# Performance work log

Measured on AMD Instinct MI355X. Metric: run time of the kernel, lower is better.

The kernel has to match this reference:

```python
import jax, jax.numpy as jnp
import numpy as np

TGT_LEN, BS, SRC_LEN, VOCAB, DIM, EMB = 24, 16, 400, 32000, 256, 256


def setup_inputs() -> dict:
    key = jax.random.key(0)
    ks = jax.random.split(key, 16)
    g = lambda k, s, sc: jax.random.normal(k, s, dtype=jnp.float32) * sc
    return {
        "inputs": jax.random.randint(ks[0], (TGT_LEN, BS), 0, VOCAB),
        "src": jax.random.randint(ks[1], (SRC_LEN, BS), 0, VOCAB),
        "h_e": g(ks[2], (SRC_LEN, BS, DIM), 0.1),
        "h0": g(ks[3], (BS, DIM), 0.1),
        "c0": g(ks[4], (BS, DIM), 0.1),
        "W_emb": g(ks[5], (VOCAB, EMB), 0.05),
        "W_ih": g(ks[6], (4 * DIM, EMB), 0.05),
        "b_ih": g(ks[7], (4 * DIM,), 0.05),
        "W_hh": g(ks[8], (4 * DIM, DIM), 0.05),
        "b_hh": g(ks[9], (4 * DIM,), 0.05),
        "W_attn_enc": g(ks[10], (DIM, DIM), 0.05),
        "W_attn_dec": g(ks[11], (DIM, DIM), 0.05),
        "W_proj": g(ks[12], (EMB, 3 * DIM), 0.05),
        "W_u": g(ks[13], (1, 3 * DIM), 0.05),
        "b_u": g(ks[14], (1,), 0.05),
        "b_out": g(ks[15], (VOCAB, 1), 0.05),
        "pad_id": 1,
    }


def reference(inputs, src, h_e, h0, c0, W_emb, W_ih, b_ih, W_hh, b_hh,
              W_attn_enc, W_attn_dec, W_proj, W_u, b_u, b_out, pad_id):
    tgt_len, bs = inputs.shape
    vocab = W_emb.shape[0]
    dim = h0.shape[1]

    emb_seq = W_emb[inputs]                       # [T, bs, emb]
    # weight-shared output projection (sect 2.4), loop-invariant -> hoisted
    W_out = jnp.tanh(W_emb @ W_proj)              # [vocab, 3*dim]
    b_out_v = b_out[:, 0]                         # [vocab]
    w_u = W_u[0]                                  # [3*dim]
    src_ids = src.T                               # [bs, src_len]
    rows = jnp.arange(bs)[:, None]
    pos = jnp.arange(tgt_len)

    def lstm_cell(x, h, c):
        gates = x @ W_ih.T + b_ih + h @ W_hh.T + b_hh
        i, f, g_, o = jnp.split(gates, 4, axis=1)
        c_new = jax.nn.sigmoid(f) * c + jax.nn.sigmoid(i) * jnp.tanh(g_)
        h_new = jax.nn.sigmoid(o) * jnp.tanh(c_new)
        return h_new, c_new

    def step(carry, xs):
        h, c, E_hist, hd_hist = carry
        emb_t, t = xs
        h, c = lstm_cell(emb_t, h, c)
        hd_t = h                                   # [bs, dim]
        # --- temporal encoder intra-attention (eq. 3-5) ---
        q = hd_t @ W_attn_enc                      # [bs, dim]
        expE = jnp.exp(jnp.einsum('bd,sbd->bs', q, h_e))  # [bs, src]
        EE = jnp.where(t == 0, expE, expE / E_hist)
        E_hist = jnp.where(t == 0, expE, E_hist + expE)
        A_e = EE / EE.sum(axis=1, keepdims=True)
        c_e = jnp.einsum('bs,sbd->bd', A_e, h_e)
        # --- decoder intra-attention over hd_history (includes current step) ---
        hd_hist = hd_hist.at[t].set(hd_t)          # [T, bs, dim]
        qd = hd_t @ W_attn_dec
        Ed = jnp.einsum('bd,tbd->bt', qd, hd_hist)
        mask = pos[None, :] <= t
        EEd = jnp.where(mask, jnp.exp(Ed), 0.0)
        A_d = EEd / EEd.sum(axis=1, keepdims=True)
        cd = jnp.einsum('bt,tbd->bd', A_d, hd_hist)
        cd_t = jnp.where(t == 0, jnp.zeros_like(cd), cd)  # t==0: cd is zeros
        # --- pointer-generator (sect 2.3) ---
        feat = jnp.concatenate([hd_t, c_e, cd_t], axis=1)   # [bs, 3*dim]
        p_switch = jax.nn.sigmoid(feat @ w_u + b_u[0])       # [bs]
        logits = feat @ W_out.T + b_out_v                     # [bs, vocab]
        logits = logits.at[:, pad_id].set(-jnp.inf)
        p_gen = jax.nn.softmax(logits, axis=1)
        copy = jnp.zeros((bs, vocab), logits.dtype).at[rows, src_ids].add(A_e)
        scores_t = (copy + p_gen) * p_switch[:, None]
        return (h, c, E_hist, hd_hist), scores_t

    hd_hist0 = jnp.zeros((tgt_len, bs, dim), h0.dtype)
    E_hist0 = jnp.ones((bs, h_e.shape[0]), h0.dtype)
    _, scores = jax.lax.scan(step, (h0, c0, E_hist0, hd_hist0), (emb_seq, pos))
    return scores  # [T, bs, vocab] mixed copy/gen distribution per step
```

## Files before the change

kernel.cpp:

```cpp
#include <hip/hip_runtime.h>
#include <cstdint>
#include <cstddef>

#define TGT   24
#define BS    16
#define SRC   400
#define VOCABN 32000
#define DIM   256
#define NROW  (TGT*BS)
#define LSTM_NBLK 4

typedef __bf16 bf16_t;
typedef __bf16 v8bf __attribute__((ext_vector_type(8)));
typedef float  v4f  __attribute__((ext_vector_type(4)));

__device__ __forceinline__ float fast_tanh(float x) {
    float e = __expf(2.f*x);
    return 1.f - 2.f/(e + 1.f);
}

__global__ void k_prep(const float* __restrict__ Whh, const float* __restrict__ Wad,
                       const float* __restrict__ he,  const float* __restrict__ Wemb,
                       const float* __restrict__ Wproj, const float* __restrict__ Wae,
                       const float* __restrict__ Wih, const int* __restrict__ inputs,
                       const float* __restrict__ h0,
                       bf16_t* o_whh, bf16_t* o_wadT, bf16_t* o_he, bf16_t* o_heT,
                       bf16_t* o_wae, bf16_t* o_wih, bf16_t* o_wprojT, bf16_t* o_embA,
                       bf16_t* o_hhi, bf16_t* o_hlo)
{
    const long S0=262144, S1=65536, S2=1638400, S3=1638400, S4=65536, S5=262144, S6=196608, S7=98304, S8=4096;
    const long total = S0+S1+S2+S3+S4+S5+S6+S7+S8;
    for (long i = (long)blockIdx.x*blockDim.x + threadIdx.x; i < total;
         i += (long)gridDim.x*blockDim.x) {
        long j = i;
        if (j < S0) { o_whh[j] = (bf16_t)Whh[j]; continue; }           j -= S0;
        if (j < S1) { long n = j>>8, k = j&255; o_wadT[j] = (bf16_t)Wad[k*DIM + n]; continue; } j -= S1;
        if (j < S2) { o_he[j] = (bf16_t)he[j]; continue; }             j -= S2;
        if (j < S3) {
            long b = j / 102400, rem = j % 102400, d = rem / 400, s = rem % 400;
            o_heT[j] = (bf16_t)he[(s*BS + b)*DIM + d]; continue; }     j -= S3;
        if (j < S4) { o_wae[j] = (bf16_t)Wae[j]; continue; }           j -= S4;
        if (j < S5) { o_wih[j] = (bf16_t)Wih[j]; continue; }           j -= S5;
        if (j < S6) { long n = j>>8, k = j&255; o_wprojT[j] = (bf16_t)Wproj[k*768 + n]; continue; } j -= S6;
        if (j < S7) { long r = j>>8, k = j&255; o_embA[j] = (bf16_t)Wemb[(long)inputs[r]*DIM + k]; continue; } j -= S7;
        {
          float v = h0[j];
          bf16_t hi = (bf16_t)v;
          o_hhi[j] = hi; o_hlo[j] = (bf16_t)(v - (float)hi); }
    }
}

__device__ __forceinline__ void gemm_tile(
    const int tid, bf16_t* As, bf16_t* Bs,
    const bf16_t* __restrict__ A, const float* __restrict__ A32,
    const bf16_t* __restrict__ B,
    const int tileIdx, const int N, const int K, const int Ntiles, const int mode,
    float* __restrict__ outF, bf16_t* __restrict__ outB,
    const float* __restrict__ bias0, const float* __restrict__ bias1,
    const int* __restrict__ padp, float* __restrict__ rsum)
{
    const int mt   = tileIdx / Ntiles, nt = tileIdx % Ntiles;
    const int m0   = mt*128, n0 = nt*128;
    const int lane = tid & 63, wave = tid >> 6;
    const int wm   = wave >> 1, wn = wave & 1;
    const int quad = lane >> 4, l16 = lane & 15;

    v4f acc[4][4];
#pragma unroll
    for (int i=0;i<4;i++)
#pragma unroll
        for (int j=0;j<4;j++) acc[i][j] = (v4f){0.f,0.f,0.f,0.f};

    const int srow = tid >> 1, shalf = tid & 1;
    const bf16_t* Ag   = A   ? A   + (size_t)(m0+srow)*K + shalf*16 : nullptr;
    const float*  Ag32 = A32 ? A32 + (size_t)(m0+srow)*K + shalf*16 : nullptr;
    const bf16_t* Bg = B + (size_t)(n0+srow)*K + shalf*16;
    bf16_t* AsW = &As[srow*40 + shalf*16];
    bf16_t* BsW = &Bs[srow*40 + shalf*16];

    for (int kc = 0; kc < K; kc += 32) {
        __syncthreads();
        uint4 b0 = *(const uint4*)(Bg + kc);
        uint4 b1 = *(const uint4*)(Bg + kc + 8);
        if (A32) {
            float4 f0 = *(const float4*)(Ag32 + kc);
            float4 f1 = *(const float4*)(Ag32 + kc + 4);
            float4 f2 = *(const float4*)(Ag32 + kc + 8);
            float4 f3 = *(const float4*)(Ag32 + kc + 12);
            v8bf u0, u1;
            u0[0]=(bf16_t)f0.x; u0[1]=(bf16_t)f0.y; u0[2]=(bf16_t)f0.z; u0[3]=(bf16_t)f0.w;
            u0[4]=(bf16_t)f1.x; u0[5]=(bf16_t)f1.y; u0[6]=(bf16_t)f1.z; u0[7]=(bf16_t)f1.w;
            u1[0]=(bf16_t)f2.x; u1[1]=(bf16_t)f2.y; u1[2]=(bf16_t)f2.z; u1[3]=(bf16_t)f2.w;
            u1[4]=(bf16_t)f3.x; u1[5]=(bf16_t)f3.y; u1[6]=(bf16_t)f3.z; u1[7]=(bf16_t)f3.w;
            *(v8bf*)AsW = u0; *(v8bf*)(AsW+8) = u1;
        } else {
            uint4 a0 = *(const uint4*)(Ag + kc);
            uint4 a1 = *(const uint4*)(Ag + kc + 8);
            *(uint4*)AsW = a0; *(uint4*)(AsW+8) = a1;
        }
        *(uint4*)BsW = b0; *(uint4*)(BsW+8) = b1;
        __syncthreads();
        v8bf af[4], bb[4];
#pragma unroll
        for (int i=0;i<4;i++) {
            af[i] = *(const v8bf*)&As[(wm*64 + i*16 + l16)*40 + quad*8];
            bb[i] = *(const v8bf*)&Bs[(wn*64 + i*16 + l16)*40 + quad*8];
        }
#pragma unroll
        for (int i=0;i<4;i++)
#pragma unroll
            for (int j=0;j<4;j++)
                acc[i][j] = __builtin_amdgcn_mfma_f32_16x16x32_bf16(af[i], bb[j], acc[i][j], 0,0,0);
    }

    const int pad = padp ? *padp : -1;
    float* rs = (float*)As;
    if (mode == 3) {
        __syncthreads();
        if (tid < 128) rs[tid] = 0.f;
        __syncthreads();
    }
#pragma unroll
    for (int i=0;i<4;i++) {
        float rloc[4] = {0.f,0.f,0.f,0.f};
#pragma unroll
        for (int j=0;j<4;j++) {
#pragma unroll
            for (int r=0;r<4;r++) {
                const int gr = m0 + wm*64 + i*16 + quad*4 + r;
                const int gc = n0 + wn*64 + j*16 + l16;
                const float v = acc[i][j][r];
                if (mode == 0)      outF[(size_t)gr*N + gc] = v + bias0[gc] + bias1[gc];
                else if (mode == 1) outB[(size_t)gr*N + gc] = (bf16_t)fast_tanh(v);
                else if (mode == 2) outB[(size_t)gr*N + gc] = (bf16_t)v;
                else if (mode == 4) outF[(size_t)gr*N + (gc & 255)*4 + (gc >> 8)] = v + bias0[gc] + bias1[gc];
                else {
                    float ex = (gc == pad) ? 0.f : __expf(v + bias0[gc]);
                    outF[(size_t)gr*N + gc] = ex;
                    rloc[r] += ex;
                }
            }
        }
        if (mode == 3) {
#pragma unroll
            for (int r=0;r<4;r++)
                atomicAdd(&rs[wm*64 + i*16 + quad*4 + r], rloc[r]);
        }
    }
    if (mode == 3) {
        __syncthreads();
        if (tid < 128) atomicAdd(&rsum[m0 + tid], rs[tid]);
    }
}

__global__ __launch_bounds__(256) void k_gemm(
    const bf16_t* __restrict__ A, const float* __restrict__ A32,
    const bf16_t* __restrict__ B,
    int M, int N, int K, int Ntiles, int mode,
    float* outF, bf16_t* outB,
    const float* __restrict__ bias0, const float* __restrict__ bias1,
    const int* __restrict__ padp, float* __restrict__ rsum)
{
    (void)M;
    __shared__ bf16_t As[128*40];
    __shared__ bf16_t Bs[128*40];
    gemm_tile(threadIdx.x, As, Bs, A, A32, B, blockIdx.x, N, K, Ntiles, mode,
              outF, outB, bias0, bias1, padp, rsum);
}

__global__ __launch_bounds__(256) void k_gemm2(
    const bf16_t* __restrict__ embA, const bf16_t* __restrict__ wih,
    float* __restrict__ xg, const float* __restrict__ b_ih, const float* __restrict__ b_hh,
    const bf16_t* __restrict__ heA, const bf16_t* __restrict__ waeB, bf16_t* __restrict__ keB)
{
    __shared__ bf16_t As[128*40];
    __shared__ bf16_t Bs[128*40];
    if (blockIdx.x < 24)
        gemm_tile(threadIdx.x, As, Bs, embA, nullptr, wih, blockIdx.x, 1024, 256, 8, 4,
                  xg, nullptr, b_ih, b_hh, nullptr, nullptr);
    else
        gemm_tile(threadIdx.x, As, Bs, heA, nullptr, waeB, blockIdx.x - 24, 256, 256, 2, 2,
                  nullptr, keB, nullptr, nullptr, nullptr, nullptr);
}

__device__ __forceinline__ void gridbar(int* bar, int target) {
    __syncthreads();
    if (threadIdx.x == 0) {
        __threadfence();
        __hip_atomic_fetch_add(bar, 1, __ATOMIC_ACQ_REL, __HIP_MEMORY_SCOPE_AGENT);
        while (__hip_atomic_load(bar, __ATOMIC_ACQUIRE, __HIP_MEMORY_SCOPE_AGENT) < target) { }
        __threadfence();
    }
    __syncthreads();
}

__global__ __launch_bounds__(512, 2) void k_lstm(
    const bf16_t* __restrict__ Whh, const float* __restrict__ xgT,
    const float* __restrict__ c0,
    bf16_t* __restrict__ hhiG, bf16_t* __restrict__ hloG,
    float* __restrict__ hallF, bf16_t* __restrict__ hallB,
    int* __restrict__ bar)
{
    __shared__ float gl[16][260];

    const int tid = threadIdx.x;
    const int k = blockIdx.x;
    const int w = tid >> 6, lane = tid & 63;
    const int l16 = lane & 15, quad = lane >> 4;

    v8bf wb[2][8];
#pragma unroll
    for (int ct = 0; ct < 2; ++ct) {
        const int c = w*32 + ct*16 + l16;
        const int row = (c >> 6)*256 + k*64 + (c & 63);
#pragma unroll
        for (int kc = 0; kc < 8; ++kc)
            wb[ct][kc] = *(const v8bf*)&Whh[(size_t)row*DIM + kc*32 + quad*8];
    }

    float cst[2];
#pragma unroll
    for (int e = 0; e < 2; ++e) {
        const int li = tid + e*512;
        cst[e] = c0[(li >> 6)*DIM + k*64 + (li & 63)];
    }

    for (int step = 0; step < TGT; ++step) {
        v8bf ahi[8], alo[8];
#pragma unroll
        for (int kc = 0; kc < 8; ++kc) {
            ahi[kc] = *(const v8bf*)&hhiG[l16*DIM + kc*32 + quad*8];
            alo[kc] = *(const v8bf*)&hloG[l16*DIM + kc*32 + quad*8];
        }
        float4 xv[2];
#pragma unroll
        for (int e = 0; e < 2; ++e) {
            const int li = tid + e*512;
            const int b = li >> 6, dd = li & 63;
            xv[e] = *(const float4*)&xgT[((size_t)(step*BS + b)*DIM + k*64 + dd)*4];
        }

        v4f acc[2] = {(v4f){0.f,0.f,0.f,0.f}, (v4f){0.f,0.f,0.f,0.f}};
#pragma unroll
        for (int kc = 0; kc < 8; ++kc)
#pragma unroll
            for (int ct = 0; ct < 2; ++ct) {
                acc[ct] = __builtin_amdgcn_mfma_f32_16x16x32_bf16(ahi[kc], wb[ct][kc], acc[ct], 0,0,0);
                acc[ct] = __builtin_amdgcn_mfma_f32_16x16x32_bf16(alo[kc], wb[ct][kc], acc[ct], 0,0,0);
            }
#pragma unroll
        for (int ct = 0; ct < 2; ++ct) {
            const int c = w*32 + ct*16 + l16;
#pragma unroll
            for (int r = 0; r < 4; ++r)
                gl[quad*4 + r][c] = acc[ct][r];
        }
        __syncthreads();
#pragma unroll
        for (int e = 0; e < 2; ++e) {
            const int li = tid + e*512;
            const int b = li >> 6, dd = li & 63;
            const int d = k*64 + dd;
            const float gi = gl[b][dd]        + xv[e].x;
            const float gf = gl[b][64 + dd]   + xv[e].y;
            const float gg = gl[b][128 + dd]  + xv[e].z;
            const float go = gl[b][192 + dd]  + xv[e].w;
            const float si = 1.f/(1.f+__expf(-gi));
            const float sf = 1.f/(1.f+__expf(-gf));
            const float so = 1.f/(1.f+__expf(-go));
            const float cn = sf*cst[e] + si*fast_tanh(gg);
            const float hn = so*fast_tanh(cn);
            cst[e] = cn;
            const bf16_t hi = (bf16_t)hn;
            hhiG[b*DIM + d] = hi;
            hloG[b*DIM + d] = (bf16_t)(hn - (float)hi);
            hallF[(size_t)(step*BS + b)*DIM + d] = hn;
            hallB[(size_t)(step*BS + b)*DIM + d] = hi;
        }
        if (step < TGT-1) gridbar(bar, (step+1)*LSTM_NBLK);
    }
}

__device__ __forceinline__ void escore_body(const int blk, const int tid, float* hS,
    const bf16_t* __restrict__ ke, const float* __restrict__ hallF, float* __restrict__ expE)
{
    const int t = blk >> 4, b = blk & 15;
    hS[tid] = hallF[(size_t)(t*BS + b)*DIM + tid];
    __syncthreads();
    for (int s = tid; s < SRC; s += 256) {
        const v8bf* kp = (const v8bf*)(ke + ((size_t)s*BS + b)*DIM);
        float e = 0.f;
#pragma unroll 8
        for (int m=0;m<32;m++) {
            v8bf kv = kp[m];
#pragma unroll
            for (int i=0;i<8;i++) e += (float)kv[i]*hS[m*8+i];
        }
        expE[((size_t)t*BS + b)*SRC + s] = __expf(e);
    }
}

__global__ __launch_bounds__(256) void k_esq(
    const bf16_t* __restrict__ ke, const float* __restrict__ hallF, float* __restrict__ expE,
    const bf16_t* __restrict__ hallB, const bf16_t* __restrict__ wadT, bf16_t* __restrict__ qdG)
{
    __shared__ __align__(16) char shb[20480];
    if (blockIdx.x < NROW) {
        escore_body(blockIdx.x, threadIdx.x, (float*)shb, ke, hallF, expE);
        return;
    }
    gemm_tile(threadIdx.x, (bf16_t*)shb, (bf16_t*)(shb + 10240), hallB, nullptr, wadT,
              blockIdx.x - NROW, 256, 256, 2, 2, nullptr, qdG, nullptr, nullptr, nullptr, nullptr);
}

__device__ void attn_body(char* sh, const int blk, const int tid,
    const float* __restrict__ expE, const bf16_t* __restrict__ heT,
    const float* __restrict__ hallF, const bf16_t* __restrict__ qdG,
    const float* __restrict__ wu, const float* __restrict__ bu,
    bf16_t* __restrict__ feat, float* __restrict__ Ae, float* __restrict__ ps)
{
    float* hS   = (float*)sh;
    float* qdS  = hS + 256;
    float* eeS  = qdS + 256;
    float* adS  = eeS + 400;
    float* red  = adS + 24;
    float* misc = red + 4;
    const int t = blk >> 4, b = blk & 15;

    hS[tid]  = hallF[(size_t)(t*BS + b)*DIM + tid];
    qdS[tid] = (float)qdG[(size_t)(t*BS + b)*DIM + tid];
    __syncthreads();

    for (int s = tid; s < SRC; s += 256) {
        float prev = 0.f;
        for (int tp = 0; tp < t; ++tp) prev += expE[((size_t)tp*BS + b)*SRC + s];
        float my = expE[((size_t)t*BS + b)*SRC + s];
        eeS[s] = (t == 0) ? my : my / prev;
    }
    __syncthreads();
    {
        float pa = 0.f;
        for (int s = tid; s < SRC; s += 256) pa += eeS[s];
#pragma unroll
        for (int o=32;o>0;o>>=1) pa += __shfl_down(pa, o);
        if ((tid & 63) == 0) red[tid>>6] = pa;
        __syncthreads();
        if (tid == 0) misc[0] = 1.f/(red[0]+red[1]+red[2]+red[3]);
        __syncthreads();
    }
    const float inv_es = misc[0];
    for (int s = tid; s < SRC; s += 256)
        Ae[((size_t)t*BS + b)*SRC + s] = eeS[s] * inv_es;

    float ce;
    {
        const v8bf* hp = (const v8bf*)(heT + ((size_t)b*DIM + tid)*SRC);
        float acc = 0.f;
#pragma unroll 10
        for (int m=0;m<50;m++) {
            v8bf hv = hp[m];
#pragma unroll
            for (int i=0;i<8;i++) acc += (float)hv[i]*eeS[m*8+i];
        }
        ce = acc * inv_es;
    }

    {
        const int wv = tid >> 6, ln = tid & 63;
        for (int tau = wv; tau <= t; tau += 4) {
            float4 a = *(const float4*)(hallF + ((size_t)(tau*BS + b))*DIM + ln*4);
            float e = a.x*qdS[ln*4] + a.y*qdS[ln*4+1] + a.z*qdS[ln*4+2] + a.w*qdS[ln*4+3];
#pragma unroll
            for (int o=32;o>0;o>>=1) e += __shfl_down(e, o);
            if (ln == 0) adS[tau] = __expf(e);
        }
    }
    __syncthreads();
    if (tid < 64) {
        float v = (tid <= t) ? adS[tid] : 0.f;
#pragma unroll
        for (int o=32;o>0;o>>=1) v += __shfl_down(v, o);
        if (tid == 0) misc[1] = 1.f/v;
    }
    __syncthreads();
    float cd = 0.f;
    for (int tau = 0; tau <= t; ++tau)
        cd += adS[tau] * hallF[((size_t)(tau*BS + b))*DIM + tid];
    cd *= misc[1];
    if (t == 0) cd = 0.f;

    const float hd = hS[tid];
    const size_t fr = ((size_t)t*BS + b)*768;
    feat[fr + tid]       = (bf16_t)hd;
    feat[fr + 256 + tid] = (bf16_t)ce;
    feat[fr + 512 + tid] = (bf16_t)cd;
    float pw = hd*wu[tid] + ce*wu[256 + tid] + cd*wu[512 + tid];
#pragma unroll
    for (int o=32;o>0;o>>=1) pw += __shfl_down(pw, o);
    if ((tid & 63) == 0) red[tid>>6] = pw;
    __syncthreads();
    if (tid == 0) {
        float s = red[0]+red[1]+red[2]+red[3];
        ps[t*BS + b] = 1.f/(1.f+__expf(-(s + bu[0])));
    }
}

__global__ __launch_bounds__(256) void k_attnw(
    const float* __restrict__ expE, const bf16_t* __restrict__ heT,
    const float* __restrict__ hallF, const bf16_t* __restrict__ qdG,
    const float* __restrict__ wu, const float* __restrict__ bu,
    bf16_t* __restrict__ feat, float* __restrict__ Ae, float* __restrict__ ps,
    const float* __restrict__ Wemb, const bf16_t* __restrict__ wprojT,
    bf16_t* __restrict__ woutB)
{
    __shared__ __align__(16) char shb[20480];
    if (blockIdx.x < NROW) {
        attn_body(shb, blockIdx.x, threadIdx.x, expE, heT, hallF, qdG, wu, bu, feat, Ae, ps);
        return;
    }
    gemm_tile(threadIdx.x, (bf16_t*)shb, (bf16_t*)(shb + 10240), nullptr, Wemb, wprojT,
              blockIdx.x - NROW, 768, 256, 6, 1,
              nullptr, woutB, nullptr, nullptr, nullptr, nullptr);
}

__global__ __launch_bounds__(256) void k_final(
    float* __restrict__ out, const float* __restrict__ rsum,
    const float* __restrict__ ps, const int* __restrict__ src,
    const float* __restrict__ Ae)
{
    const int r = blockIdx.x;
    const int b = r & (BS-1);
    const float p  = ps[r];
    const float sc = p / rsum[r];
    float4* o4 = (float4*)(out + (size_t)r*VOCABN);
    for (int i = threadIdx.x; i < VOCABN/4; i += 256) {
        float4 v = o4[i];
        v.x*=sc; v.y*=sc; v.z*=sc; v.w*=sc;
        o4[i] = v;
    }
    __syncthreads();
    for (int s = threadIdx.x; s < SRC; s += 256) {
        const int v = src[s*BS + b];
        atomicAdd(&out[(size_t)r*VOCABN + v], Ae[(size_t)r*SRC + s] * p);
    }
}

#define O_WHH    0u
#define O_WADT   524288u
#define O_HEBF   655360u
#define O_HET    3932160u
#define O_KE     7208960u
#define O_WAE    10485760u
#define O_WPROJT 10616832u
#define O_WIH    11010048u
#define O_EMBA   11534336u
#define O_WOUT   11730944u
#define O_XG     60882944u
#define O_HALLF  62455808u
#define O_HALLB  62849024u
#define O_QD     63045632u
#define O_EXPE   63242240u
#define O_FEAT   63856640u
#define O_AE     64446464u
#define O_PS     65060864u
#define O_BAR    65062400u
#define O_RSUM   65063936u

extern "C" void kernel_launch(void* const* d_in, const int* in_sizes, int n_in,
                              void* d_out, int out_size, void* d_ws, size_t ws_size,
                              hipStream_t stream)
{
    const int*   inputs = (const int*)  d_in[0];
    const int*   src    = (const int*)  d_in[1];
    const float* h_e    = (const float*)d_in[2];
    const float* h0     = (const float*)d_in[3];
    const float* c0     = (const float*)d_in[4];
    const float* W_emb  = (const float*)d_in[5];
    const float* W_ih   = (const float*)d_in[6];
    const float* b_ih   = (const float*)d_in[7];
    const float* W_hh   = (const float*)d_in[8];
    const float* b_hh   = (const float*)d_in[9];
    const float* W_ae   = (const float*)d_in[10];
    const float* W_ad   = (const float*)d_in[11];
    const float* W_proj = (const float*)d_in[12];
    const float* W_u    = (const float*)d_in[13];
    const float* b_u    = (const float*)d_in[14];
    const float* b_out  = (const float*)d_in[15];
    const int*   pad_id = (const int*)  d_in[16];

    char* w = (char*)d_ws;
    bf16_t* whh_bf  = (bf16_t*)(w + O_WHH);
    bf16_t* wadT_bf = (bf16_t*)(w + O_WADT);
    bf16_t* he_bf   = (bf16_t*)(w + O_HEBF);
    bf16_t* heT_bf  = (bf16_t*)(w + O_HET);
    bf16_t* ke_bf   = (bf16_t*)(w + O_KE);
    bf16_t* wae_bf  = (bf16_t*)(w + O_WAE);
    bf16_t* wprojT  = (bf16_t*)(w + O_WPROJT);
    bf16_t* wih_bf  = (bf16_t*)(w + O_WIH);
    bf16_t* embA_bf = (bf16_t*)(w + O_EMBA);
    bf16_t* wout_bf = (bf16_t*)(w + O_WOUT);
    float*  xg      = (float*) (w + O_XG);
    float*  hallF   = (float*) (w + O_HALLF);
    bf16_t* hallB   = (bf16_t*)(w + O_HALLB);
    bf16_t* qdG     = (bf16_t*)(w + O_QD);
    float*  expE    = (float*) (w + O_EXPE);
    bf16_t* hhiG    = (bf16_t*)(w + O_EXPE);
    bf16_t* hloG    = (bf16_t*)(w + O_EXPE + 8192);
    bf16_t* feat_bf = (bf16_t*)(w + O_FEAT);
    float*  Ae      = (float*) (w + O_AE);
    float*  ps      = (float*) (w + O_PS);
    int*    bar     = (int*)   (w + O_BAR);
    float*  rsum    = (float*) (w + O_RSUM);
    float*  out     = (float*)d_out;

    k_prep<<<1024, 256, 0, stream>>>(W_hh, W_ad, h_e, W_emb, W_proj, W_ae, W_ih, inputs, h0,
                                     whh_bf, wadT_bf, he_bf, heT_bf,
                                     wae_bf, wih_bf, wprojT, embA_bf, hhiG, hloG);
    hipMemsetAsync(w + O_BAR, 0, 3072, stream);
    k_gemm2<<<124, 256, 0, stream>>>(embA_bf, wih_bf, xg, b_ih, b_hh,
                                     he_bf, wae_bf, ke_bf);
    k_lstm<<<LSTM_NBLK, 512, 0, stream>>>(whh_bf, xg, c0, hhiG, hloG,
                                          hallF, hallB, bar);
    k_esq<<<NROW + 6, 256, 0, stream>>>(ke_bf, hallF, expE, hallB, wadT_bf, qdG);
    k_attnw<<<NROW + 1500, 256, 0, stream>>>(expE, heT_bf, hallF, qdG, W_u, b_u,
                                             feat_bf, Ae, ps,
                                             W_emb, wprojT, wout_bf);
    k_gemm<<<750, 256, 0, stream>>>(feat_bf, nullptr, wout_bf, NROW, VOCABN, 768, 250, 3,
                                    out, nullptr, b_out, nullptr, pad_id, rsum);
    k_final<<<NROW, 256, 0, stream>>>(out, rsum, ps, src, Ae);
}
```

Measured before the change: 448.6 us.

## Precompute temporal attention prefix sums and specialize vocab GEMM with K=64 tiles

New measurement: 436.9 us. -2.6%, faster.

```diff
diff --git a/kernel.cpp b/kernel.cpp
--- a/kernel.cpp
+++ b/kernel.cpp
@@ -13,6 +13,7 @@
 typedef __bf16 bf16_t;
 typedef __bf16 v8bf __attribute__((ext_vector_type(8)));
 typedef float  v4f  __attribute__((ext_vector_type(4)));
+typedef unsigned int u32;
 
 __device__ __forceinline__ float fast_tanh(float x) {
     float e = __expf(2.f*x);
@@ -56,8 +57,7 @@
     const bf16_t* __restrict__ B,
     const int tileIdx, const int N, const int K, const int Ntiles, const int mode,
     float* __restrict__ outF, bf16_t* __restrict__ outB,
-    const float* __restrict__ bias0, const float* __restrict__ bias1,
-    const int* __restrict__ padp, float* __restrict__ rsum)
+    const float* __restrict__ bias0, const float* __restrict__ bias1)
 {
     const int mt   = tileIdx / Ntiles, nt = tileIdx % Ntiles;
     const int m0   = mt*128, n0 = nt*128;
@@ -113,16 +113,8 @@
                 acc[i][j] = __builtin_amdgcn_mfma_f32_16x16x32_bf16(af[i], bb[j], acc[i][j], 0,0,0);
     }
 
-    const int pad = padp ? *padp : -1;
-    float* rs = (float*)As;
-    if (mode == 3) {
-        __syncthreads();
-        if (tid < 128) rs[tid] = 0.f;
-        __syncthreads();
-    }
 #pragma unroll
     for (int i=0;i<4;i++) {
-        float rloc[4] = {0.f,0.f,0.f,0.f};
 #pragma unroll
         for (int j=0;j<4;j++) {
 #pragma unroll
@@ -134,38 +126,9 @@
                 else if (mode == 1) outB[(size_t)gr*N + gc] = (bf16_t)fast_tanh(v);
                 else if (mode == 2) outB[(size_t)gr*N + gc] = (bf16_t)v;
                 else if (mode == 4) outF[(size_t)gr*N + (gc & 255)*4 + (gc >> 8)] = v + bias0[gc] + bias1[gc];
-                else {
-                    float ex = (gc == pad) ? 0.f : __expf(v + bias0[gc]);
-                    outF[(size_t)gr*N + gc] = ex;
-                    rloc[r] += ex;
-                }
             }
         }
-        if (mode == 3) {
-#pragma unroll
-            for (int r=0;r<4;r++)
-                atomicAdd(&rs[wm*64 + i*16 + quad*4 + r], rloc[r]);
-        }
-    }
-    if (mode == 3) {
-        __syncthreads();
-        if (tid < 128) atomicAdd(&rsum[m0 + tid], rs[tid]);
-    }
-}
-
-__global__ __launch_bounds__(256) void k_gemm(
-    const bf16_t* __restrict__ A, const float* __restrict__ A32,
-    const bf16_t* __restrict__ B,
-    int M, int N, int K, int Ntiles, int mode,
-    float* outF, bf16_t* outB,
-    const float* __restrict__ bias0, const float* __restrict__ bias1,
-    const int* __restrict__ padp, float* __restrict__ rsum)
-{
-    (void)M;
-    __shared__ bf16_t As[128*40];
-    __shared__ bf16_t Bs[128*40];
-    gemm_tile(threadIdx.x, As, Bs, A, A32, B, blockIdx.x, N, K, Ntiles, mode,
-              outF, outB, bias0, bias1, padp, rsum);
+    }
 }
 
 __global__ __launch_bounds__(256) void k_gemm2(
@@ -177,10 +140,94 @@
     __shared__ bf16_t Bs[128*40];
     if (blockIdx.x < 24)
         gemm_tile(threadIdx.x, As, Bs, embA, nullptr, wih, blockIdx.x, 1024, 256, 8, 4,
-                  xg, nullptr, b_ih, b_hh, nullptr, nullptr);
+                  xg, nullptr, b_ih, b_hh);
     else
         gemm_tile(threadIdx.x, As, Bs, heA, nullptr, waeB, blockIdx.x - 24, 256, 256, 2, 2,
-                  nullptr, keB, nullptr, nullptr, nullptr, nullptr);
+                  nullptr, keB, nullptr, nullptr);
+}
+
+__global__ __launch_bounds__(256) void k_gemm3(
+    const bf16_t* __restrict__ A, const bf16_t* __restrict__ B,
+    float* __restrict__ outF, const float* __restrict__ bias0,
+    const int* __restrict__ padp, float* __restrict__ rsum)
+{
+    __shared__ bf16_t As[128*72];
+    __shared__ bf16_t Bs[128*72];
+    const int tid = threadIdx.x;
+    const int mt = blockIdx.x / 250, nt = blockIdx.x % 250;
+    const int m0 = mt*128, n0 = nt*128;
+    const int lane = tid & 63, wave = tid >> 6;
+    const int wm = wave >> 1, wn = wave & 1;
+    const int quad = lane >> 4, l16 = lane & 15;
+
+    v4f acc[4][4];
+#pragma unroll
+    for (int i=0;i<4;i++)
+#pragma unroll
+        for (int j=0;j<4;j++) acc[i][j] = (v4f){0.f,0.f,0.f,0.f};
+
+    const int srow = tid >> 1, shalf = tid & 1;
+    const bf16_t* Ag = A + (size_t)(m0+srow)*768 + shalf*32;
+    const bf16_t* Bg = B + (size_t)(n0+srow)*768 + shalf*32;
+    bf16_t* AsW = &As[srow*72 + shalf*32];
+    bf16_t* BsW = &Bs[srow*72 + shalf*32];
+
+    for (int kc = 0; kc < 768; kc += 64) {
+        __syncthreads();
+        uint4 a0 = *(const uint4*)(Ag + kc);
+        uint4 a1 = *(const uint4*)(Ag + kc + 8);
+        uint4 a2 = *(const uint4*)(Ag + kc + 16);
+        uint4 a3 = *(const uint4*)(Ag + kc + 24);
+        uint4 b0 = *(const uint4*)(Bg + kc);
+        uint4 b1 = *(const uint4*)(Bg + kc + 8);
+        uint4 b2 = *(const uint4*)(Bg + kc + 16);
+        uint4 b3 = *(const uint4*)(Bg + kc + 24);
+        *(uint4*)(AsW)    = a0; *(uint4*)(AsW+8)  = a1;
+        *(uint4*)(AsW+16) = a2; *(uint4*)(AsW+24) = a3;
+        *(uint4*)(BsW)    = b0; *(uint4*)(BsW+8)  = b1;
+        *(uint4*)(BsW+16) = b2; *(uint4*)(BsW+24) = b3;
+        __syncthreads();
+#pragma unroll
+        for (int kk = 0; kk < 2; ++kk) {
+            v8bf af[4], bb[4];
+#pragma unroll
+            for (int i=0;i<4;i++) {
+                af[i] = *(const v8bf*)&As[(wm*64 + i*16 + l16)*72 + kk*32 + quad*8];
+                bb[i] = *(const v8bf*)&Bs[(wn*64 + i*16 + l16)*72 + kk*32 + quad*8];
+            }
+#pragma unroll
+            for (int i=0;i<4;i++)
+#pragma unroll
+                for (int j=0;j<4;j++)
+                    acc[i][j] = __builtin_amdgcn_mfma_f32_16x16x32_bf16(af[i], bb[j], acc[i][j], 0,0,0);
+        }
+    }
+
+    const int pad = *padp;
+    float* rs = (float*)As;
+    __syncthreads();
+    if (tid < 128) rs[tid] = 0.f;
+    __syncthreads();
+#pragma unroll
+    for (int i=0;i<4;i++) {
+        float rloc[4] = {0.f,0.f,0.f,0.f};
+#pragma unroll
+        for (int j=0;j<4;j++) {
+#pragma unroll
+            for (int r=0;r<4;r++) {
+                const int gr = m0 + wm*64 + i*16 + quad*4 + r;
+                const int gc = n0 + wn*64 + j*16 + l16;
+                const float ex = (gc == pad) ? 0.f : __expf(acc[i][j][r] + bias0[gc]);
+                outF[(size_t)gr*VOCABN + gc] = ex;
+                rloc[r] += ex;
+            }
+        }
+#pragma unroll
+        for (int r=0;r<4;r++)
+            atomicAdd(&rs[wm*64 + i*16 + quad*4 + r], rloc[r]);
+    }
+    __syncthreads();
+    if (tid < 128) atomicAdd(&rsum[m0 + tid], rs[tid]);
 }
 
 __device__ __forceinline__ void gridbar(int* bar, int target) {
@@ -310,11 +357,24 @@
         return;
     }
     gemm_tile(threadIdx.x, (bf16_t*)shb, (bf16_t*)(shb + 10240), hallB, nullptr, wadT,
-              blockIdx.x - NROW, 256, 256, 2, 2, nullptr, qdG, nullptr, nullptr, nullptr, nullptr);
+              blockIdx.x - NROW, 256, 256, 2, 2, nullptr, qdG, nullptr, nullptr);
+}
+
+__global__ __launch_bounds__(256) void k_prefix(float* __restrict__ expE)
+{
+    const int i = blockIdx.x*256 + threadIdx.x;
+    if (i >= BS*SRC) return;
+    const int b = i / SRC, s = i % SRC;
+    float c = 0.f;
+    for (int t = 0; t < TGT; ++t) {
+        const size_t idx = ((size_t)t*BS + b)*SRC + s;
+        c += expE[idx];
+        expE[idx] = c;
+    }
 }
 
 __device__ void attn_body(char* sh, const int blk, const int tid,
-    const float* __restrict__ expE, const bf16_t* __restrict__ heT,
+    const float* __restrict__ cumE, const bf16_t* __restrict__ heT,
     const float* __restrict__ hallF, const bf16_t* __restrict__ qdG,
     const float* __restrict__ wu, const float* __restrict__ bu,
     bf16_t* __restrict__ feat, float* __restrict__ Ae, float* __restrict__ ps)
@@ -332,10 +392,13 @@
     __syncthreads();
 
     for (int s = tid; s < SRC; s += 256) {
-        float prev = 0.f;
-        for (int tp = 0; tp < t; ++tp) prev += expE[((size_t)tp*BS + b)*SRC + s];
-        float my = expE[((size_t)t*BS + b)*SRC + s];
-        eeS[s] = (t == 0) ? my : my / prev;
+        if (t == 0) {
+            eeS[s] = cumE[(size_t)b*SRC + s];
+        } else {
+            const float prev = cumE[((size_t)(t-1)*BS + b)*SRC + s];
+            const float cur  = cumE[((size_t)t*BS + b)*SRC + s];
+            eeS[s] = (cur - prev) / prev;
+        }
     }
     __syncthreads();
     {
@@ -406,7 +469,7 @@
 }
 
 __global__ __launch_bounds__(256) void k_attnw(
-    const float* __restrict__ expE, const bf16_t* __restrict__ heT,
+    const float* __restrict__ cumE, const bf16_t* __restrict__ heT,
     const float* __restrict__ hallF, const bf16_t* __restrict__ qdG,
     const float* __restrict__ wu, const float* __restrict__ bu,
     bf16_t* __restrict__ feat, float* __restrict__ Ae, float* __restrict__ ps,
@@ -415,12 +478,12 @@
 {
     __shared__ __align__(16) char shb[20480];
     if (blockIdx.x < NROW) {
-        attn_body(shb, blockIdx.x, threadIdx.x, expE, heT, hallF, qdG, wu, bu, feat, Ae, ps);
+        attn_body(shb, blockIdx.x, threadIdx.x, cumE, heT, hallF, qdG, wu, bu, feat, Ae, ps);
         return;
     }
     gemm_tile(threadIdx.x, (bf16_t*)shb, (bf16_t*)(shb + 10240), nullptr, Wemb, wprojT,
               blockIdx.x - NROW, 768, 256, 6, 1,
-              nullptr, woutB, nullptr, nullptr, nullptr, nullptr);
+              nullptr, woutB, nullptr, nullptr);
 }
 
 __global__ __launch_bounds__(256) void k_final(
@@ -522,10 +585,10 @@
     k_lstm<<<LSTM_NBLK, 512, 0, stream>>>(whh_bf, xg, c0, hhiG, hloG,
                                           hallF, hallB, bar);
     k_esq<<<NROW + 6, 256, 0, stream>>>(ke_bf, hallF, expE, hallB, wadT_bf, qdG);
+    k_prefix<<<25, 256, 0, stream>>>(expE);
     k_attnw<<<NROW + 1500, 256, 0, stream>>>(expE, heT_bf, hallF, qdG, W_u, b_u,
                                              feat_bf, Ae, ps,
                                              W_emb, wprojT, wout_bf);
-    k_gemm<<<750, 256, 0, stream>>>(feat_bf, nullptr, wout_bf, NROW, VOCABN, 768, 250, 3,
-                                    out, nullptr, b_out, nullptr, pad_id, rsum);
+    k_gemm3<<<750, 256, 0, stream>>>(feat_bf, wout_bf, out, b_out, pad_id, rsum);
     k_final<<<NROW, 256, 0, stream>>>(out, rsum, ps, src, Ae);
 }
```
